# Kernel tuning notes

Measured on AMD Instinct MI355X. Metric: run time of the kernel, lower is better.

The kernel has to match this reference:

```python
import jax, jax.numpy as jnp
import numpy as np

B, L = 4096, 200
N_USERS, N_ITEMS, N_CATS, N_DUR = 200000, 500000, 1000, 20
D = 64  # item_embed_dim == seq_embed_dim


def _lin(k, din, dout):
    kw, kb = jax.random.split(k)
    s = 1.0 / np.sqrt(din)
    return (jax.random.uniform(kw, (din, dout), minval=-s, maxval=s),
            jax.random.uniform(kb, (dout,), minval=-s, maxval=s))


def setup_inputs() -> dict:
    key = jax.random.key(0)
    ks = jax.random.split(key, 20)
    inp = {
        'user_id': jax.random.randint(ks[0], (B,), 0, N_USERS),
        'item_id': jax.random.randint(ks[1], (B,), 0, N_ITEMS),
        'item_category': jax.random.randint(ks[2], (B,), 0, N_CATS),
        'item_dur_bkt': jax.random.randint(ks[3], (B,), 0, N_DUR),
        'user_dense': jax.random.normal(ks[4], (B, 25), dtype=jnp.float32),
        'item_dense': jax.random.normal(ks[5], (B, 3), dtype=jnp.float32),
        'history_seq': jax.random.randint(ks[6], (B, L), 0, N_ITEMS + 1),
        # embedding tables (init std=0.01 as in _init_weights)
        'user_W': 0.01 * jax.random.normal(ks[7], (N_USERS, 64), dtype=jnp.float32),
        'item_W': 0.01 * jax.random.normal(ks[8], (N_ITEMS, D), dtype=jnp.float32),
        'cat_W': 0.01 * jax.random.normal(ks[9], (N_CATS, 16), dtype=jnp.float32),
        'dur_W': 0.01 * jax.random.normal(ks[10], (N_DUR, 8), dtype=jnp.float32),
        'hist_W': 0.01 * jax.random.normal(ks[11], (N_ITEMS + 1, D), dtype=jnp.float32),
    }
    # attention MLP: 4*D=256 -> 64 -> 32 -> 1
    inp['aW0'], inp['ab0'] = _lin(ks[12], 4 * D, 64)
    inp['aW1'], inp['ab1'] = _lin(ks[13], 64, 32)
    inp['aW2'], inp['ab2'] = _lin(ks[14], 32, 1)
    # final MLP: concat_dim 64+64+16+8+25+3+64 = 244 -> 256 -> 128 -> 1
    inp['mW0'], inp['mb0'] = _lin(ks[15], 244, 256)
    inp['mW1'], inp['mb1'] = _lin(ks[16], 256, 128)
    inp['mW2'], inp['mb2'] = _lin(ks[17], 128, 1)
    return inp


def reference(user_id, item_id, item_category, item_dur_bkt, user_dense, item_dense,
              history_seq, user_W, item_W, cat_W, dur_W, hist_W,
              aW0, ab0, aW1, ab1, aW2, ab2, mW0, mb0, mW1, mb1, mW2, mb2):
    u_emb = user_W[user_id]            # (B, 64)
    i_emb = item_W[item_id]            # (B, D)
    c_emb = cat_W[item_category]       # (B, 16)
    d_emb = dur_W[item_dur_bkt]        # (B, 8)
    hist = hist_W[history_seq]         # (B, L, D)

    t = i_emb[:, None, :]              # (B, 1, D); item_dim == seq_dim so no slice
    tb = jnp.broadcast_to(t, hist.shape)
    feat = jnp.concatenate([hist, tb, hist * t, hist - t], axis=-1)  # (B, L, 4D)

    h = jax.nn.relu(feat @ aW0 + ab0)
    h = jax.nn.relu(h @ aW1 + ab1)
    scores = (h @ aW2 + ab2)[..., 0]   # (B, L)

    pad_mask = history_seq == 0
    scores = jnp.where(pad_mask, jnp.float32(-1e9), scores)
    w = jax.nn.softmax(scores, axis=-1)                # (B, L)
    pooled = jnp.einsum('bl,bld->bd', w, hist)         # (B, D)

    x = jnp.concatenate([u_emb, i_emb, c_emb, d_emb, user_dense, item_dense, pooled], axis=-1)
    h = jax.nn.relu(x @ mW0 + mb0)     # dropout is identity in eval mode
    h = jax.nn.relu(h @ mW1 + mb1)
    logit = (h @ mW2 + mb2)[..., 0]
    return jax.nn.sigmoid(logit)       # (B,)
```

## Files before the change

### kernel.cpp

```cpp
#include <hip/hip_runtime.h>
#include <hip/hip_bf16.h>

#define L_SZ 200
#define RB 8
#define HS_STRIDE 72

typedef __attribute__((ext_vector_type(8))) short short8;
typedef __attribute__((ext_vector_type(4))) float floatx4;

__device__ __forceinline__ unsigned short f2bf(float f) {
    unsigned int u = __float_as_uint(f);
    unsigned int r = (u + 0x7fffu + ((u >> 16) & 1u)) >> 16;
    return (unsigned short)r;
}
__device__ __forceinline__ float bf2f(unsigned short h) {
    return __uint_as_float(((unsigned int)h) << 16);
}
__device__ __forceinline__ float wave_sum64(float v) {
    #pragma unroll
    for (int m = 1; m <= 32; m <<= 1) v += __shfl_xor(v, m, 64);
    return v;
}
__device__ __forceinline__ float wave_max64(float v) {
    #pragma unroll
    for (int m = 1; m <= 32; m <<= 1) v = fmaxf(v, __shfl_xor(v, m, 64));
    return v;
}
__device__ __forceinline__ unsigned int pk2(float a, float b) {
    return ((unsigned int)f2bf(b) << 16) | (unsigned int)f2bf(a);
}

__global__ __launch_bounds__(256) void attn_kernel(
    const int* __restrict__ item_id, const int* __restrict__ hist_seq,
    const float* __restrict__ item_W, const float* __restrict__ hist_W,
    const float* __restrict__ aW0, const float* __restrict__ ab0,
    const float* __restrict__ aW1, const float* __restrict__ ab1,
    const float* __restrict__ aW2, const float* __restrict__ ab2,
    float* __restrict__ pooled_ws)
{
    __shared__ __align__(16) unsigned char smem[53664];
    unsigned short* Hs  = (unsigned short*)(smem);
    unsigned short* WeT = (unsigned short*)(smem + 29952);
    unsigned short* W1T = (unsigned short*)(smem + 38144);
    unsigned short* scr = (unsigned short*)(smem + 42240);
    float* pools        = (float*)(smem + 42240);
    float* scores       = (float*)(smem + 51456);
    float* iemb         = (float*)(smem + 52288);
    float* cb           = (float*)(smem + 52544);
    int*   seq_sh       = (int*)(smem + 52800);
    float* red          = (float*)(smem + 53632);

    const int tid  = threadIdx.x;
    const int w    = tid >> 6;
    const int lane = tid & 63;
    const int b    = blockIdx.x;
    const int* hseq = hist_seq + b * L_SZ;

    if (tid < 64)  iemb[tid]   = item_W[(size_t)item_id[b] * 64 + tid];
    if (tid < 208) seq_sh[tid] = (tid < L_SZ) ? hseq[tid] : 0;
    __syncthreads();

    for (int u = tid; u < 208 * 8; u += 256) {
        int row = u >> 3, c8 = u & 7;
        float4 f0 = {0.f,0.f,0.f,0.f}, f1 = {0.f,0.f,0.f,0.f};
        if (row < L_SZ) {
            const float* src = hist_W + (size_t)seq_sh[row] * 64 + c8 * 8;
            f0 = *(const float4*)src;
            f1 = *(const float4*)(src + 4);
        }
        uint4 pk;
        pk.x = pk2(f0.x, f0.y); pk.y = pk2(f0.z, f0.w);
        pk.z = pk2(f1.x, f1.y); pk.w = pk2(f1.z, f1.w);
        *(uint4*)(Hs + row * HS_STRIDE + c8 * 8) = pk;
    }

    for (int u = tid; u < 512; u += 256) {
        int j = u >> 3, k8 = u & 7;
        float4 ie0 = *(const float4*)&iemb[k8 * 8];
        float4 ie1 = *(const float4*)&iemb[k8 * 8 + 4];
        float ie[8] = {ie0.x, ie0.y, ie0.z, ie0.w, ie1.x, ie1.y, ie1.z, ie1.w};
        float v[8];
        #pragma unroll
        for (int i = 0; i < 8; ++i) {
            int k = k8 * 8 + i;
            v[i] = aW0[k * 64 + j] + aW0[(192 + k) * 64 + j]
                 + ie[i] * aW0[(128 + k) * 64 + j];
        }
        uint4 pk;
        pk.x = pk2(v[0], v[1]); pk.y = pk2(v[2], v[3]);
        pk.z = pk2(v[4], v[5]); pk.w = pk2(v[6], v[7]);
        *(uint4*)(WeT + j * 64 + k8 * 8) = pk;
    }

    {
        int n = tid >> 3, k8 = tid & 7;
        float v[8];
        #pragma unroll
        for (int i = 0; i < 8; ++i) v[i] = aW1[(k8 * 8 + i) * 32 + n];
        uint4 pk;
        pk.x = pk2(v[0], v[1]); pk.y = pk2(v[2], v[3]);
        pk.z = pk2(v[4], v[5]); pk.w = pk2(v[6], v[7]);
        *(uint4*)(W1T + n * 64 + k8 * 8) = pk;
    }

    {
        float cpart = 0.f;
        #pragma unroll 4
        for (int t = 0; t < 16; ++t) {
            int k = w * 16 + t;
            cpart = fmaf(iemb[k], aW0[(64 + k) * 64 + lane] - aW0[(192 + k) * 64 + lane], cpart);
        }
        pools[w * 64 + lane] = cpart;
    }
    __syncthreads();
    if (tid < 64)
        cb[tid] = ab0[tid] + ((pools[tid] + pools[64 + tid]) + (pools[128 + tid] + pools[192 + tid]));
    __syncthreads();

    const int c = lane & 15, q = lane >> 4;
    short8 bW[4][2], bW1[2][2];
    #pragma unroll
    for (int nt = 0; nt < 4; ++nt)
        #pragma unroll
        for (int ks = 0; ks < 2; ++ks)
            bW[nt][ks] = *(const short8*)(WeT + (nt * 16 + c) * 64 + ks * 32 + q * 8);
    #pragma unroll
    for (int nt = 0; nt < 2; ++nt)
        #pragma unroll
        for (int ks = 0; ks < 2; ++ks)
            bW1[nt][ks] = *(const short8*)(W1T + (nt * 16 + c) * 64 + ks * 32 + q * 8);
    float cbr[4];
    #pragma unroll
    for (int nt = 0; nt < 4; ++nt) cbr[nt] = cb[nt * 16 + c];
    float ab1r[2], aw2r[2];
    #pragma unroll
    for (int nt = 0; nt < 2; ++nt) {
        ab1r[nt] = ab1[nt * 16 + c];
        aw2r[nt] = aW2[nt * 16 + c];
    }
    const float ab2s = ab2[0];
    unsigned short* scrw = scr + w * (16 * HS_STRIDE);
    const floatx4 zf = {0.f, 0.f, 0.f, 0.f};

    for (int mt = w; mt < 13; mt += 4) {
        const int rowbase = mt * 16;
        floatx4 acc0[4] = {zf, zf, zf, zf};
        #pragma unroll
        for (int ks = 0; ks < 2; ++ks) {
            short8 a = *(const short8*)(Hs + (rowbase + c) * HS_STRIDE + ks * 32 + q * 8);
            acc0[0] = __builtin_amdgcn_mfma_f32_16x16x32_bf16(a, bW[0][ks], acc0[0], 0, 0, 0);
            acc0[1] = __builtin_amdgcn_mfma_f32_16x16x32_bf16(a, bW[1][ks], acc0[1], 0, 0, 0);
            acc0[2] = __builtin_amdgcn_mfma_f32_16x16x32_bf16(a, bW[2][ks], acc0[2], 0, 0, 0);
            acc0[3] = __builtin_amdgcn_mfma_f32_16x16x32_bf16(a, bW[3][ks], acc0[3], 0, 0, 0);
        }
        #pragma unroll
        for (int nt = 0; nt < 4; ++nt)
            #pragma unroll
            for (int r = 0; r < 4; ++r) {
                float h = fmaxf(acc0[nt][r] + cbr[nt], 0.f);
                scrw[(q * 4 + r) * HS_STRIDE + nt * 16 + c] = f2bf(h);
            }
        floatx4 acc1[2] = {zf, zf};
        #pragma unroll
        for (int ks = 0; ks < 2; ++ks) {
            short8 a1 = *(const short8*)(scrw + c * HS_STRIDE + ks * 32 + q * 8);
            acc1[0] = __builtin_amdgcn_mfma_f32_16x16x32_bf16(a1, bW1[0][ks], acc1[0], 0, 0, 0);
            acc1[1] = __builtin_amdgcn_mfma_f32_16x16x32_bf16(a1, bW1[1][ks], acc1[1], 0, 0, 0);
        }
        float s[4];
        #pragma unroll
        for (int r = 0; r < 4; ++r)
            s[r] = fmaxf(acc1[0][r] + ab1r[0], 0.f) * aw2r[0]
                 + fmaxf(acc1[1][r] + ab1r[1], 0.f) * aw2r[1];
        #pragma unroll
        for (int m = 1; m <= 8; m <<= 1)
            #pragma unroll
            for (int r = 0; r < 4; ++r) s[r] += __shfl_xor(s[r], m, 64);
        if (c == 0) {
            #pragma unroll
            for (int r = 0; r < 4; ++r) {
                int l = rowbase + q * 4 + r;
                if (l < L_SZ)
                    scores[l] = (seq_sh[l] == 0) ? -1.0e9f : (s[r] + ab2s);
            }
        }
    }
    __syncthreads();

    float s0 = (tid < L_SZ) ? scores[tid] : -3.0e38f;
    float mx = wave_max64(s0);
    if (lane == 0) red[w] = mx;
    __syncthreads();
    mx = fmaxf(fmaxf(red[0], red[1]), fmaxf(red[2], red[3]));
    float e = (tid < L_SZ) ? __expf(s0 - mx) : 0.f;
    float sm = wave_sum64(e);
    if (lane == 0) red[4 + w] = sm;
    __syncthreads();
    const float winv = 1.f / ((red[4] + red[5]) + (red[6] + red[7]));
    if (tid < L_SZ) scores[tid] = e * winv;
    __syncthreads();

    {
        int g  = (w << 1) | (lane >> 5);
        int jj = lane & 31;
        int l0 = g * 26, l1 = (l0 + 26 < L_SZ) ? l0 + 26 : L_SZ;
        float p0 = 0.f, p1 = 0.f;
        for (int l = l0; l < l1; ++l) {
            float wt = scores[l];
            unsigned int pv = *(const unsigned int*)(Hs + l * HS_STRIDE + jj * 2);
            p0 = fmaf(wt, bf2f((unsigned short)(pv & 0xffffu)), p0);
            p1 = fmaf(wt, bf2f((unsigned short)(pv >> 16)), p1);
        }
        float2 pp = {p0, p1};
        *(float2*)&pools[g * 64 + jj * 2] = pp;
    }
    __syncthreads();
    if (tid < 64) {
        float sum = 0.f;
        #pragma unroll
        for (int g = 0; g < 8; ++g) sum += pools[g * 64 + tid];
        pooled_ws[(size_t)b * 64 + tid] = sum;
    }
}

__global__ __launch_bounds__(256) void mlp_kernel(
    const int* __restrict__ user_id, const int* __restrict__ item_id,
    const int* __restrict__ item_cat, const int* __restrict__ item_dur,
    const float* __restrict__ user_dense, const float* __restrict__ item_dense,
    const float* __restrict__ user_W, const float* __restrict__ item_W,
    const float* __restrict__ cat_W, const float* __restrict__ dur_W,
    const float* __restrict__ mW0, const float* __restrict__ mb0,
    const float* __restrict__ mW1, const float* __restrict__ mb1,
    const float* __restrict__ mW2, const float* __restrict__ mb2,
    const float* __restrict__ pooled_ws, float* __restrict__ out)
{
    __shared__ __align__(16) float xT[244][RB];
    __shared__ __align__(16) float h0T[256][RB];
    __shared__ __align__(16) float h1T[128][RB];
    __shared__ __align__(16) float part[128][RB];

    const int tid = threadIdx.x;
    const int b0 = blockIdx.x * RB;

    for (int idx = tid; idx < 244 * RB; idx += 256) {
        int r = idx / 244;
        int c = idx - r * 244;
        int b = b0 + r;
        float v;
        if (c < 64)       v = user_W[(size_t)user_id[b] * 64 + c];
        else if (c < 128) v = item_W[(size_t)item_id[b] * 64 + (c - 64)];
        else if (c < 144) v = cat_W[item_cat[b] * 16 + (c - 128)];
        else if (c < 152) v = dur_W[item_dur[b] * 8 + (c - 144)];
        else if (c < 177) v = user_dense[b * 25 + (c - 152)];
        else if (c < 180) v = item_dense[b * 3 + (c - 177)];
        else              v = pooled_ws[(size_t)b * 64 + (c - 180)];
        xT[c][r] = v;
    }
    __syncthreads();

    {
        float acc[RB];
        const float bias = mb0[tid];
        #pragma unroll
        for (int r = 0; r < RB; ++r) acc[r] = bias;
        #pragma unroll 4
        for (int k = 0; k < 244; ++k) {
            float wk = mW0[k * 256 + tid];
            float4 xa = *(const float4*)&xT[k][0];
            float4 xb = *(const float4*)&xT[k][4];
            acc[0] = fmaf(wk, xa.x, acc[0]);
            acc[1] = fmaf(wk, xa.y, acc[1]);
            acc[2] = fmaf(wk, xa.z, acc[2]);
            acc[3] = fmaf(wk, xa.w, acc[3]);
            acc[4] = fmaf(wk, xb.x, acc[4]);
            acc[5] = fmaf(wk, xb.y, acc[5]);
            acc[6] = fmaf(wk, xb.z, acc[6]);
            acc[7] = fmaf(wk, xb.w, acc[7]);
        }
        #pragma unroll
        for (int r = 0; r < RB; ++r) h0T[tid][r] = fmaxf(acc[r], 0.f);
    }
    __syncthreads();

    const int jj = tid & 127;
    const int half = tid >> 7;
    {
        float acc[RB];
        #pragma unroll
        for (int r = 0; r < RB; ++r) acc[r] = 0.f;
        #pragma unroll 4
        for (int t = 0; t < 128; ++t) {
            int k = half * 128 + t;
            float wk = mW1[k * 128 + jj];
            float4 ha = *(const float4*)&h0T[k][0];
            float4 hb = *(const float4*)&h0T[k][4];
            acc[0] = fmaf(wk, ha.x, acc[0]);
            acc[1] = fmaf(wk, ha.y, acc[1]);
            acc[2] = fmaf(wk, ha.z, acc[2]);
            acc[3] = fmaf(wk, ha.w, acc[3]);
            acc[4] = fmaf(wk, hb.x, acc[4]);
            acc[5] = fmaf(wk, hb.y, acc[5]);
            acc[6] = fmaf(wk, hb.z, acc[6]);
            acc[7] = fmaf(wk, hb.w, acc[7]);
        }
        if (half == 1) {
            #pragma unroll
            for (int r = 0; r < RB; ++r) part[jj][r] = acc[r];
        }
        __syncthreads();
        if (half == 0) {
            const float bias = mb1[jj];
            #pragma unroll
            for (int r = 0; r < RB; ++r)
                h1T[jj][r] = fmaxf(acc[r] + part[jj][r] + bias, 0.f);
        }
    }
    __syncthreads();

    if (tid < RB) {
        const int r = tid;
        float a0 = mb2[0], a1 = 0.f;
        #pragma unroll 8
        for (int k = 0; k < 128; k += 2) {
            a0 = fmaf(h1T[k][r],     mW2[k],     a0);
            a1 = fmaf(h1T[k + 1][r], mW2[k + 1], a1);
        }
        float a = a0 + a1;
        out[b0 + r] = 1.f / (1.f + __expf(-a));
    }
}

extern "C" void kernel_launch(void* const* d_in, const int* in_sizes, int n_in,
                              void* d_out, int out_size, void* d_ws, size_t ws_size,
                              hipStream_t stream) {
    (void)in_sizes; (void)n_in; (void)out_size; (void)ws_size;
    const int*   user_id    = (const int*)d_in[0];
    const int*   item_id    = (const int*)d_in[1];
    const int*   item_cat   = (const int*)d_in[2];
    const int*   item_dur   = (const int*)d_in[3];
    const float* user_dense = (const float*)d_in[4];
    const float* item_dense = (const float*)d_in[5];
    const int*   hist_seq   = (const int*)d_in[6];
    const float* user_W     = (const float*)d_in[7];
    const float* item_W     = (const float*)d_in[8];
    const float* cat_W      = (const float*)d_in[9];
    const float* dur_W      = (const float*)d_in[10];
    const float* hist_W     = (const float*)d_in[11];
    const float* aW0 = (const float*)d_in[12];
    const float* ab0 = (const float*)d_in[13];
    const float* aW1 = (const float*)d_in[14];
    const float* ab1 = (const float*)d_in[15];
    const float* aW2 = (const float*)d_in[16];
    const float* ab2 = (const float*)d_in[17];
    const float* mW0 = (const float*)d_in[18];
    const float* mb0 = (const float*)d_in[19];
    const float* mW1 = (const float*)d_in[20];
    const float* mb1 = (const float*)d_in[21];
    const float* mW2 = (const float*)d_in[22];
    const float* mb2 = (const float*)d_in[23];
    float* out = (float*)d_out;
    float* pooled_ws = (float*)d_ws;

    attn_kernel<<<4096, 256, 0, stream>>>(item_id, hist_seq, item_W, hist_W,
                                          aW0, ab0, aW1, ab1, aW2, ab2, pooled_ws);
    mlp_kernel<<<4096 / RB, 256, 0, stream>>>(user_id, item_id, item_cat, item_dur,
                                              user_dense, item_dense,
                                              user_W, item_W, cat_W, dur_W,
                                              mW0, mb0, mW1, mb1, mW2, mb2,
                                              pooled_ws, out);
}
```

Baseline: 451.4 us.

## Shrink LDS footprint with buffer aliasing and swizzle to raise block occupancy

Cuts shared memory per block from about 53.7KB to about 39KB and sets launch bounds to 4 blocks per SM. It does this by dropping the padding rows of the history tile, aliasing the weight tile, the per-wave scratch and the pools into one buffer, and loading aW1 straight into registers. XOR swizzling replaces the padded row stride for the weight and scratch tiles so LDS accesses avoid bank conflicts. The aim is more resident blocks to hide the latency of the random embedding gathers. The cost is an extra barrier and a tighter register budget, which could cause spills.

```diff
diff --git a/kernel.cpp b/kernel.cpp
--- a/kernel.cpp
+++ b/kernel.cpp
@@ -30,7 +30,7 @@
     return ((unsigned int)f2bf(b) << 16) | (unsigned int)f2bf(a);
 }
 
-__global__ __launch_bounds__(256) void attn_kernel(
+__global__ __launch_bounds__(256, 4) void attn_kernel(
     const int* __restrict__ item_id, const int* __restrict__ hist_seq,
     const float* __restrict__ item_W, const float* __restrict__ hist_W,
     const float* __restrict__ aW0, const float* __restrict__ ab0,
@@ -38,17 +38,14 @@
     const float* __restrict__ aW2, const float* __restrict__ ab2,
     float* __restrict__ pooled_ws)
 {
-    __shared__ __align__(16) unsigned char smem[53664];
+    __shared__ __align__(16) unsigned char smem[39136];
     unsigned short* Hs  = (unsigned short*)(smem);
-    unsigned short* WeT = (unsigned short*)(smem + 29952);
-    unsigned short* W1T = (unsigned short*)(smem + 38144);
-    unsigned short* scr = (unsigned short*)(smem + 42240);
-    float* pools        = (float*)(smem + 42240);
-    float* scores       = (float*)(smem + 51456);
-    float* iemb         = (float*)(smem + 52288);
-    float* cb           = (float*)(smem + 52544);
-    int*   seq_sh       = (int*)(smem + 52800);
-    float* red          = (float*)(smem + 53632);
+    unsigned short* BB  = (unsigned short*)(smem + 28800);
+    int*   seq_sh = (int*)(smem + 36992);
+    float* scores = (float*)(smem + 37792);
+    float* iemb   = (float*)(smem + 38592);
+    float* cb     = (float*)(smem + 38848);
+    float* red    = (float*)(smem + 39104);
 
     const int tid  = threadIdx.x;
     const int w    = tid >> 6;
@@ -56,82 +53,55 @@
     const int b    = blockIdx.x;
     const int* hseq = hist_seq + b * L_SZ;
 
-    if (tid < 64)  iemb[tid]   = item_W[(size_t)item_id[b] * 64 + tid];
-    if (tid < 208) seq_sh[tid] = (tid < L_SZ) ? hseq[tid] : 0;
-    __syncthreads();
-
-    for (int u = tid; u < 208 * 8; u += 256) {
+    if (tid < 64)   iemb[tid]   = item_W[(size_t)item_id[b] * 64 + tid];
+    if (tid < L_SZ) seq_sh[tid] = hseq[tid];
+    __syncthreads();
+
+    for (int u = tid; u < L_SZ * 8; u += 256) {
         int row = u >> 3, c8 = u & 7;
-        float4 f0 = {0.f,0.f,0.f,0.f}, f1 = {0.f,0.f,0.f,0.f};
-        if (row < L_SZ) {
-            const float* src = hist_W + (size_t)seq_sh[row] * 64 + c8 * 8;
-            f0 = *(const float4*)src;
-            f1 = *(const float4*)(src + 4);
-        }
+        const float* src = hist_W + (size_t)seq_sh[row] * 64 + c8 * 8;
+        float4 f0 = *(const float4*)src;
+        float4 f1 = *(const float4*)(src + 4);
         uint4 pk;
         pk.x = pk2(f0.x, f0.y); pk.y = pk2(f0.z, f0.w);
         pk.z = pk2(f1.x, f1.y); pk.w = pk2(f1.z, f1.w);
         *(uint4*)(Hs + row * HS_STRIDE + c8 * 8) = pk;
     }
-
     for (int u = tid; u < 512; u += 256) {
         int j = u >> 3, k8 = u & 7;
-        float4 ie0 = *(const float4*)&iemb[k8 * 8];
-        float4 ie1 = *(const float4*)&iemb[k8 * 8 + 4];
-        float ie[8] = {ie0.x, ie0.y, ie0.z, ie0.w, ie1.x, ie1.y, ie1.z, ie1.w};
         float v[8];
         #pragma unroll
         for (int i = 0; i < 8; ++i) {
             int k = k8 * 8 + i;
             v[i] = aW0[k * 64 + j] + aW0[(192 + k) * 64 + j]
-                 + ie[i] * aW0[(128 + k) * 64 + j];
+                 + iemb[k] * aW0[(128 + k) * 64 + j];
         }
         uint4 pk;
         pk.x = pk2(v[0], v[1]); pk.y = pk2(v[2], v[3]);
         pk.z = pk2(v[4], v[5]); pk.w = pk2(v[6], v[7]);
-        *(uint4*)(WeT + j * 64 + k8 * 8) = pk;
-    }
-
-    {
-        int n = tid >> 3, k8 = tid & 7;
-        float v[8];
-        #pragma unroll
-        for (int i = 0; i < 8; ++i) v[i] = aW1[(k8 * 8 + i) * 32 + n];
-        uint4 pk;
-        pk.x = pk2(v[0], v[1]); pk.y = pk2(v[2], v[3]);
-        pk.z = pk2(v[4], v[5]); pk.w = pk2(v[6], v[7]);
-        *(uint4*)(W1T + n * 64 + k8 * 8) = pk;
-    }
-
-    {
+        *(uint4*)(BB + j * 64 + (k8 ^ (j & 7)) * 8) = pk;
+    }
+    if (w < 2) {
         float cpart = 0.f;
         #pragma unroll 4
-        for (int t = 0; t < 16; ++t) {
-            int k = w * 16 + t;
+        for (int t = 0; t < 32; ++t) {
+            int k = w * 32 + t;
             cpart = fmaf(iemb[k], aW0[(64 + k) * 64 + lane] - aW0[(192 + k) * 64 + lane], cpart);
         }
-        pools[w * 64 + lane] = cpart;
-    }
-    __syncthreads();
-    if (tid < 64)
-        cb[tid] = ab0[tid] + ((pools[tid] + pools[64 + tid]) + (pools[128 + tid] + pools[192 + tid]));
-    __syncthreads();
-
+        scores[w * 64 + lane] = cpart;
+    }
     const int c = lane & 15, q = lane >> 4;
-    short8 bW[4][2], bW1[2][2];
-    #pragma unroll
-    for (int nt = 0; nt < 4; ++nt)
-        #pragma unroll
-        for (int ks = 0; ks < 2; ++ks)
-            bW[nt][ks] = *(const short8*)(WeT + (nt * 16 + c) * 64 + ks * 32 + q * 8);
+    short8 bW1[2][2];
     #pragma unroll
     for (int nt = 0; nt < 2; ++nt)
         #pragma unroll
-        for (int ks = 0; ks < 2; ++ks)
-            bW1[nt][ks] = *(const short8*)(W1T + (nt * 16 + c) * 64 + ks * 32 + q * 8);
-    float cbr[4];
-    #pragma unroll
-    for (int nt = 0; nt < 4; ++nt) cbr[nt] = cb[nt * 16 + c];
+        for (int ks = 0; ks < 2; ++ks) {
+            unsigned short tmp[8];
+            #pragma unroll
+            for (int i = 0; i < 8; ++i)
+                tmp[i] = f2bf(aW1[(ks * 32 + q * 8 + i) * 32 + nt * 16 + c]);
+            bW1[nt][ks] = *(short8*)tmp;
+        }
     float ab1r[2], aw2r[2];
     #pragma unroll
     for (int nt = 0; nt < 2; ++nt) {
@@ -139,7 +109,23 @@
         aw2r[nt] = aW2[nt * 16 + c];
     }
     const float ab2s = ab2[0];
-    unsigned short* scrw = scr + w * (16 * HS_STRIDE);
+    __syncthreads();
+
+    short8 bW[4][2];
+    #pragma unroll
+    for (int nt = 0; nt < 4; ++nt)
+        #pragma unroll
+        for (int ks = 0; ks < 2; ++ks)
+            bW[nt][ks] = *(const short8*)(BB + (nt * 16 + c) * 64
+                                             + ((4 * ks + q) ^ (c & 7)) * 8);
+    if (tid < 64)
+        cb[tid] = ab0[tid] + scores[tid] + scores[64 + tid];
+    __syncthreads();
+
+    float cbr[4];
+    #pragma unroll
+    for (int nt = 0; nt < 4; ++nt) cbr[nt] = cb[nt * 16 + c];
+    unsigned short* scrw = BB + w * (16 * 64);
     const floatx4 zf = {0.f, 0.f, 0.f, 0.f};
 
     for (int mt = w; mt < 13; mt += 4) {
@@ -158,12 +144,14 @@
             #pragma unroll
             for (int r = 0; r < 4; ++r) {
                 float h = fmaxf(acc0[nt][r] + cbr[nt], 0.f);
-                scrw[(q * 4 + r) * HS_STRIDE + nt * 16 + c] = f2bf(h);
+                int row = q * 4 + r;
+                int gp = (2 * nt + (c >> 3)) ^ (row & 7);
+                scrw[row * 64 + gp * 8 + (c & 7)] = f2bf(h);
             }
         floatx4 acc1[2] = {zf, zf};
         #pragma unroll
         for (int ks = 0; ks < 2; ++ks) {
-            short8 a1 = *(const short8*)(scrw + c * HS_STRIDE + ks * 32 + q * 8);
+            short8 a1 = *(const short8*)(scrw + c * 64 + ((4 * ks + q) ^ (c & 7)) * 8);
             acc1[0] = __builtin_amdgcn_mfma_f32_16x16x32_bf16(a1, bW1[0][ks], acc1[0], 0, 0, 0);
             acc1[1] = __builtin_amdgcn_mfma_f32_16x16x32_bf16(a1, bW1[1][ks], acc1[1], 0, 0, 0);
         }
@@ -200,6 +188,7 @@
     if (tid < L_SZ) scores[tid] = e * winv;
     __syncthreads();
 
+    float* pools = (float*)BB;
     {
         int g  = (w << 1) | (lane >> 5);
         int jj = lane & 31;
```

Result: faster. 431.2 us (-4.5%).
